# Kernel optimization log

Hardware: AMD Instinct MI355X
Metric: run time of the kernel (lower is better)

The kernel has to match this reference:

```python
import jax, jax.numpy as jnp
import numpy as np

THETA0 = 3.0
THETA = 5.0
BIG = 1e10  # stands in for +inf in the squared-distance transform


def _edt_sq_1d(f):
    # f: [..., n] of squared distances; returns min_j (i-j)^2 + f[j] per i.
    n = f.shape[-1]
    i = jnp.arange(n, dtype=f.dtype)
    d2 = (i[:, None] - i[None, :]) ** 2  # [n, n]
    return jnp.min(f[..., None, :] + d2, axis=-1)


def _edt(mask):
    # Exact Euclidean distance from each voxel to the nearest zero of `mask`
    # (matches scipy.ndimage.distance_transform_edt on a binary mask),
    # via the separable squared-distance transform applied axis by axis.
    f = jnp.where(mask > 0.5, jnp.asarray(BIG, mask.dtype), jnp.asarray(0.0, mask.dtype))
    for ax in range(1, mask.ndim):  # skip batch axis 0
        f = jnp.moveaxis(_edt_sq_1d(jnp.moveaxis(f, ax, -1)), -1, ax)
    return jnp.sqrt(f)


def setup_inputs() -> dict:
    key = jax.random.key(0)
    k1, k2 = jax.random.split(key)
    B, D, H, W = 2, 64, 96, 96
    pred = jax.random.uniform(k1, (B, D, H, W), dtype=jnp.float32)  # probabilities
    target = jax.random.randint(k2, (B, D, H, W), 0, 2).astype(jnp.float32)  # binary mask
    return {"pred": pred, "target": target}


def reference(pred, target):
    # Signed distance phi = dist_to_foreground_boundary framework: 
    # dist_pos = EDT(target) (distance to nearest background voxel),
    # dist_neg = EDT(1 - target).
    dist_pos = _edt(target)
    dist_neg = _edt(1.0 - target)
    a = jnp.abs(dist_neg - dist_pos)
    w = jnp.where(
        a <= THETA0,
        1.0,
        jnp.where(a >= THETA, 0.0, 1.0 - (a - THETA0) / (THETA - THETA0)),
    )
    w = jax.lax.stop_gradient(w)  # original computes weights from detached numpy target

    # binary_cross_entropy with torch's log clamp at -100
    log_p = jnp.clip(jnp.log(pred), -100.0)
    log_1mp = jnp.clip(jnp.log(1.0 - pred), -100.0)
    bce = -(target * log_p + (1.0 - target) * log_1mp)  # [B, D, H, W]

    num = jnp.sum(bce * w, axis=(1, 2, 3))
    den = jnp.sum(w, axis=(1, 2, 3)) + 1e-5
    return jnp.mean(num / den)
```

## Files before the change

kernel.cpp:

```cpp
#include <hip/hip_runtime.h>
#include <math.h>

#define BDIM 2
#define DDIM 64
#define HDIM 96
#define WDIM 96

#define DT 8
#define HT 8
#define WT 32
#define DH 16
#define HH 16
#define NROWS (DH * HH)
#define NBLK  (BDIM * (DDIM / DT) * (HDIM / HT) * (WDIM / WT))

__global__ void init_acc(float* __restrict__ acc) {
    if (threadIdx.x < 4) acc[threadIdx.x] = 0.0f;
    if (threadIdx.x == 4) ((int*)acc)[4] = 0;
}

__device__ __forceinline__ unsigned vminu4(unsigned a, unsigned b) {
    unsigned c = ((a | 0x80808080u) - b) & 0x80808080u;
    unsigned m = (c - (c >> 7)) | c;
    return a ^ ((a ^ b) & m);
}

__device__ __forceinline__ unsigned shiftw(unsigned lo, unsigned hi, int t) {
#if __has_builtin(__builtin_amdgcn_alignbyte)
    return __builtin_amdgcn_alignbyte(hi, lo, t);
#else
    return (lo >> (8 * t)) | (hi << (32 - 8 * t));
#endif
}

__device__ __forceinline__ unsigned wpass_quad(unsigned W0, unsigned W1, unsigned W2) {
    unsigned m = 0x19191919u - W1 * 25u;
    unsigned u08 = W0 | W2;
    m = vminu4(m, 0x19191919u - u08 * 9u);
    unsigned u17 = shiftw(W0, W1, 1) | shiftw(W1, W2, 3);
    m = vminu4(m, 0x19191919u - u17 * 16u);
    unsigned u26 = shiftw(W0, W1, 2) | shiftw(W1, W2, 2);
    m = vminu4(m, 0x19191919u - u26 * 21u);
    unsigned u35 = shiftw(W0, W1, 3) | shiftw(W1, W2, 1);
    m = vminu4(m, 0x19191919u - u35 * 24u);
    return m;
}

__global__ __launch_bounds__(256) void boundary_fused(const float* __restrict__ pred,
                                                      const float* __restrict__ target,
                                                      float* __restrict__ acc,
                                                      float* __restrict__ out) {
    __shared__ unsigned fgm[NROWS * 10];
    __shared__ unsigned bgm[NROWS * 10];
    __shared__ unsigned swp[NROWS * 8];
    __shared__ unsigned swn[NROWS * 8];
    __shared__ float rsum[8];
    unsigned* whp = fgm;
    unsigned* whn = bgm;

    const int tid = threadIdx.x;
    int x = blockIdx.x;
    const int wt = x % 3;  x /= 3;
    const int ht = x % 12; x /= 12;
    const int dt = x % 8;
    const int b  = x / 8;
    const int d0 = dt * DT, h0 = ht * HT, w0 = wt * WT;

    #pragma unroll
    for (int k = 0; k < 10; ++k) {
        const int idx = tid + 256 * k;
        const int row = idx / 10;
        const int q   = idx - row * 10;
        const int dr = row >> 4, hr = row & 15;
        const int d = d0 - 4 + dr, h = h0 - 4 + hr;
        const int wb = w0 - 4 + 4 * q;
        unsigned fgw = 0u, bgw = 0u;
        if ((unsigned)d < DDIM && (unsigned)h < HDIM && (unsigned)wb < WDIM) {
            const float4 v = *(const float4*)(target +
                ((size_t)(b * DDIM + d) * HDIM + h) * WDIM + wb);
            fgw = (unsigned)(v.x > 0.5f)        | ((unsigned)(v.y > 0.5f) << 8) |
                  ((unsigned)(v.z > 0.5f) << 16) | ((unsigned)(v.w > 0.5f) << 24);
            bgw = fgw ^ 0x01010101u;
        }
        fgm[row * 10 + q] = fgw;
        bgm[row * 10 + q] = bgw;
    }
    __syncthreads();

    {
        const int qp = tid & 7;
        const int rb = tid >> 3;
        #pragma unroll
        for (int k = 0; k < 8; ++k) {
            const int row  = rb + 32 * k;
            const int base = row * 10 + qp;
            swn[row * 8 + qp] = wpass_quad(fgm[base], fgm[base + 1], fgm[base + 2]);
            swp[row * 8 + qp] = wpass_quad(bgm[base], bgm[base + 1], bgm[base + 2]);
        }
    }
    __syncthreads();

    #pragma unroll
    for (int k = 0; k < 4; ++k) {
        const int g  = tid + 256 * k;
        const int q  = g & 7;
        const int hh = (g >> 3) & 7;
        const int dr = g >> 6;
        unsigned p = 0x19191919u, n = 0x19191919u;
        #pragma unroll
        for (int t = 0; t < 9; ++t) {
            const unsigned add = (unsigned)((t - 4) * (t - 4)) * 0x01010101u;
            const int src = (dr * HH + hh + t) * 8 + q;
            p = vminu4(p, swp[src] + add);
            n = vminu4(n, swn[src] + add);
        }
        whp[(dr * HT + hh) * 8 + q] = p;
        whn[(dr * HT + hh) * 8 + q] = n;
    }
    __syncthreads();

    float num = 0.f, den = 0.f;
    #pragma unroll
    for (int k = 0; k < 2; ++k) {
        const int g  = tid + 256 * k;
        const int q  = g & 7;
        const int hh = (g >> 3) & 7;
        const int di = g >> 6;
        unsigned p = 0x19191919u, n = 0x19191919u;
        #pragma unroll
        for (int t = 0; t < 9; ++t) {
            const unsigned add = (unsigned)((t - 4) * (t - 4)) * 0x01010101u;
            const int src = ((di + t) * HT + hh) * 8 + q;
            p = vminu4(p, whp[src] + add);
            n = vminu4(n, whn[src] + add);
        }
        const size_t gg = ((size_t)(b * DDIM + d0 + di) * HDIM + h0 + hh) * WDIM
                        + w0 + q * 4;
        const float4 pr = *(const float4*)(pred + gg);
        const float4 tg = *(const float4*)(target + gg);
        #pragma unroll
        for (int j = 0; j < 4; ++j) {
            const float pv = (float)((p >> (8 * j)) & 0xFFu);
            const float nv = (float)((n >> (8 * j)) & 0xFFu);
            const float prj = j == 0 ? pr.x : j == 1 ? pr.y : j == 2 ? pr.z : pr.w;
            const float tgj = j == 0 ? tg.x : j == 1 ? tg.y : j == 2 ? tg.z : tg.w;
            const float dp = sqrtf(pv);
            const float dn = sqrtf(nv);
            const float a  = fabsf(dn - dp);
            float w;
            if (a <= 3.0f)      w = 1.0f;
            else if (a >= 5.0f) w = 0.0f;
            else                w = 1.0f - (a - 3.0f) * 0.5f;
            const float lp  = fmaxf(logf(prj), -100.0f);
            const float l1  = fmaxf(logf(1.0f - prj), -100.0f);
            const float bce = -(tgj * lp + (1.0f - tgj) * l1);
            num += bce * w;
            den += w;
        }
    }

    for (int off = 32; off > 0; off >>= 1) {
        num += __shfl_down(num, off);
        den += __shfl_down(den, off);
    }
    if ((tid & 63) == 0) {
        rsum[tid >> 6]       = num;
        rsum[4 + (tid >> 6)] = den;
    }
    __syncthreads();
    if (tid == 0) {
        float ns = rsum[0] + rsum[1] + rsum[2] + rsum[3];
        float ds = rsum[4] + rsum[5] + rsum[6] + rsum[7];
        atomicAdd(&acc[b], ns);
        atomicAdd(&acc[2 + b], ds);
        __threadfence();
        int done = atomicAdd((int*)acc + 4, 1);
        if (done == NBLK - 1) {
            __threadfence();
            float n0  = atomicAdd(&acc[0], 0.0f);
            float n1  = atomicAdd(&acc[1], 0.0f);
            float d0_ = atomicAdd(&acc[2], 0.0f);
            float d1_ = atomicAdd(&acc[3], 0.0f);
            out[0] = 0.5f * (n0 / (d0_ + 1e-5f) + n1 / (d1_ + 1e-5f));
        }
    }
}

extern "C" void kernel_launch(void* const* d_in, const int* in_sizes, int n_in,
                              void* d_out, int out_size, void* d_ws, size_t ws_size,
                              hipStream_t stream) {
    const float* pred   = (const float*)d_in[0];
    const float* target = (const float*)d_in[1];
    float* acc = (float*)d_ws;
    float* out = (float*)d_out;

    init_acc<<<1, 64, 0, stream>>>(acc);
    boundary_fused<<<NBLK, 256, 0, stream>>>(pred, target, acc, out);
}
```

Before: 94.66 us.

## Repack distance maps as 16-bit pos/neg pairs with per-row register W-pass

Each thread now loads one whole input row into registers and runs the width pass there, so the byte-mask shared arrays and one barrier go away. The results are stored as interleaved 16-bit positive/negative pairs, and the H and D passes use packed u16 min instead of the SWAR byte-min emulation. The final stage switches from float4 per-thread loads to one element per thread, coalesced across 32 columns. This removes shared-memory round trips and bit-trick ALU work, at the cost of more per-thread H/D iterations and scalar global loads.

```diff
diff --git a/kernel.cpp b/kernel.cpp
--- a/kernel.cpp
+++ b/kernel.cpp
@@ -12,7 +12,10 @@
 #define DH 16
 #define HH 16
 #define NROWS (DH * HH)
+#define SWSTR 36
 #define NBLK  (BDIM * (DDIM / DT) * (HDIM / HT) * (WDIM / WT))
+
+typedef unsigned short ushort2v __attribute__((ext_vector_type(2)));
 
 __global__ void init_acc(float* __restrict__ acc) {
     if (threadIdx.x < 4) acc[threadIdx.x] = 0.0f;
@@ -23,6 +26,12 @@
     unsigned c = ((a | 0x80808080u) - b) & 0x80808080u;
     unsigned m = (c - (c >> 7)) | c;
     return a ^ ((a ^ b) & m);
+}
+
+__device__ __forceinline__ unsigned pkmin(unsigned a, unsigned b) {
+    ushort2v r = __builtin_elementwise_min(__builtin_bit_cast(ushort2v, a),
+                                           __builtin_bit_cast(ushort2v, b));
+    return __builtin_bit_cast(unsigned, r);
 }
 
 __device__ __forceinline__ unsigned shiftw(unsigned lo, unsigned hi, int t) {
@@ -50,113 +59,99 @@
                                                       const float* __restrict__ target,
                                                       float* __restrict__ acc,
                                                       float* __restrict__ out) {
-    __shared__ unsigned fgm[NROWS * 10];
-    __shared__ unsigned bgm[NROWS * 10];
-    __shared__ unsigned swp[NROWS * 8];
-    __shared__ unsigned swn[NROWS * 8];
+    __shared__ __align__(16) unsigned swpn[NROWS * SWSTR];
+    __shared__ unsigned whpn[DH * HT * WT];
     __shared__ float rsum[8];
-    unsigned* whp = fgm;
-    unsigned* whn = bgm;
 
     const int tid = threadIdx.x;
     int x = blockIdx.x;
     const int wt = x % 3;  x /= 3;
     const int ht = x % 12; x /= 12;
     const int dt = x % 8;
-    const int b  = x / 8;
+    const int bi = x / 8;
     const int d0 = dt * DT, h0 = ht * HT, w0 = wt * WT;
 
-    #pragma unroll
-    for (int k = 0; k < 10; ++k) {
-        const int idx = tid + 256 * k;
-        const int row = idx / 10;
-        const int q   = idx - row * 10;
-        const int dr = row >> 4, hr = row & 15;
+    {
+        const int r  = tid;
+        const int dr = r >> 4, hr = r & 15;
         const int d = d0 - 4 + dr, h = h0 - 4 + hr;
-        const int wb = w0 - 4 + 4 * q;
-        unsigned fgw = 0u, bgw = 0u;
-        if ((unsigned)d < DDIM && (unsigned)h < HDIM && (unsigned)wb < WDIM) {
-            const float4 v = *(const float4*)(target +
-                ((size_t)(b * DDIM + d) * HDIM + h) * WDIM + wb);
-            fgw = (unsigned)(v.x > 0.5f)        | ((unsigned)(v.y > 0.5f) << 8) |
-                  ((unsigned)(v.z > 0.5f) << 16) | ((unsigned)(v.w > 0.5f) << 24);
-            bgw = fgw ^ 0x01010101u;
+        const bool rowvalid = ((unsigned)d < DDIM) && ((unsigned)h < HDIM);
+        const unsigned rv = rowvalid ? 0x01010101u : 0u;
+        const float* rowp = target + ((size_t)(bi * DDIM + d) * HDIM + h) * WDIM + (w0 - 4);
+
+        unsigned Wf[10], Wb[10];
+        #pragma unroll
+        for (int q = 0; q < 10; ++q) {
+            unsigned vbq = 0x01010101u;
+            if (q == 0 && wt == 0) vbq = 0u;
+            if (q == 9 && wt == 2) vbq = 0u;
+            unsigned fg = 0u;
+            if (rowvalid && vbq) {
+                const float4 v = *(const float4*)(rowp + 4 * q);
+                fg = (unsigned)(v.x > 0.5f)         | ((unsigned)(v.y > 0.5f) << 8) |
+                     ((unsigned)(v.z > 0.5f) << 16) | ((unsigned)(v.w > 0.5f) << 24);
+            }
+            Wf[q] = fg;
+            Wb[q] = (fg ^ 0x01010101u) & vbq & rv;
         }
-        fgm[row * 10 + q] = fgw;
-        bgm[row * 10 + q] = bgw;
-    }
-    __syncthreads();
-
-    {
-        const int qp = tid & 7;
-        const int rb = tid >> 3;
         #pragma unroll
-        for (int k = 0; k < 8; ++k) {
-            const int row  = rb + 32 * k;
-            const int base = row * 10 + qp;
-            swn[row * 8 + qp] = wpass_quad(fgm[base], fgm[base + 1], fgm[base + 2]);
-            swp[row * 8 + qp] = wpass_quad(bgm[base], bgm[base + 1], bgm[base + 2]);
+        for (int q = 0; q < 8; ++q) {
+            const unsigned nb = wpass_quad(Wf[q], Wf[q + 1], Wf[q + 2]);
+            const unsigned pb = wpass_quad(Wb[q], Wb[q + 1], Wb[q + 2]);
+            uint4 e;
+            e.x = (pb & 0xFFu)         | ((nb & 0xFFu) << 16);
+            e.y = ((pb >> 8) & 0xFFu)  | (((nb >> 8) & 0xFFu) << 16);
+            e.z = ((pb >> 16) & 0xFFu) | (((nb >> 16) & 0xFFu) << 16);
+            e.w = (pb >> 24)           | ((nb >> 24) << 16);
+            *(uint4*)&swpn[r * SWSTR + 4 * q] = e;
         }
     }
     __syncthreads();
 
     #pragma unroll
-    for (int k = 0; k < 4; ++k) {
-        const int g  = tid + 256 * k;
-        const int q  = g & 7;
-        const int hh = (g >> 3) & 7;
-        const int dr = g >> 6;
-        unsigned p = 0x19191919u, n = 0x19191919u;
+    for (int k = 0; k < 16; ++k) {
+        const int idx = tid + 256 * k;
+        const int c   = idx & 31;
+        const int hh  = (idx >> 5) & 7;
+        const int dr  = idx >> 8;
+        unsigned a = 0x00190019u;
         #pragma unroll
         for (int t = 0; t < 9; ++t) {
-            const unsigned add = (unsigned)((t - 4) * (t - 4)) * 0x01010101u;
-            const int src = (dr * HH + hh + t) * 8 + q;
-            p = vminu4(p, swp[src] + add);
-            n = vminu4(n, swn[src] + add);
+            const unsigned v = swpn[(dr * HH + hh + t) * SWSTR + c];
+            a = pkmin(a, v + (unsigned)((t - 4) * (t - 4)) * 0x00010001u);
         }
-        whp[(dr * HT + hh) * 8 + q] = p;
-        whn[(dr * HT + hh) * 8 + q] = n;
+        whpn[(dr * HT + hh) * WT + c] = a;
     }
     __syncthreads();
 
     float num = 0.f, den = 0.f;
     #pragma unroll
-    for (int k = 0; k < 2; ++k) {
-        const int g  = tid + 256 * k;
-        const int q  = g & 7;
-        const int hh = (g >> 3) & 7;
-        const int di = g >> 6;
-        unsigned p = 0x19191919u, n = 0x19191919u;
+    for (int k = 0; k < 8; ++k) {
+        const int idx = tid + 256 * k;
+        const int c   = idx & 31;
+        const int hh  = (idx >> 5) & 7;
+        const int di  = idx >> 8;
+        unsigned a = 0x00190019u;
         #pragma unroll
         for (int t = 0; t < 9; ++t) {
-            const unsigned add = (unsigned)((t - 4) * (t - 4)) * 0x01010101u;
-            const int src = ((di + t) * HT + hh) * 8 + q;
-            p = vminu4(p, whp[src] + add);
-            n = vminu4(n, whn[src] + add);
+            const unsigned v = whpn[((di + t) * HT + hh) * WT + c];
+            a = pkmin(a, v + (unsigned)((t - 4) * (t - 4)) * 0x00010001u);
         }
-        const size_t gg = ((size_t)(b * DDIM + d0 + di) * HDIM + h0 + hh) * WDIM
-                        + w0 + q * 4;
-        const float4 pr = *(const float4*)(pred + gg);
-        const float4 tg = *(const float4*)(target + gg);
-        #pragma unroll
-        for (int j = 0; j < 4; ++j) {
-            const float pv = (float)((p >> (8 * j)) & 0xFFu);
-            const float nv = (float)((n >> (8 * j)) & 0xFFu);
-            const float prj = j == 0 ? pr.x : j == 1 ? pr.y : j == 2 ? pr.z : pr.w;
-            const float tgj = j == 0 ? tg.x : j == 1 ? tg.y : j == 2 ? tg.z : tg.w;
-            const float dp = sqrtf(pv);
-            const float dn = sqrtf(nv);
-            const float a  = fabsf(dn - dp);
-            float w;
-            if (a <= 3.0f)      w = 1.0f;
-            else if (a >= 5.0f) w = 0.0f;
-            else                w = 1.0f - (a - 3.0f) * 0.5f;
-            const float lp  = fmaxf(logf(prj), -100.0f);
-            const float l1  = fmaxf(logf(1.0f - prj), -100.0f);
-            const float bce = -(tgj * lp + (1.0f - tgj) * l1);
-            num += bce * w;
-            den += w;
-        }
+        const size_t g = ((size_t)(bi * DDIM + d0 + di) * HDIM + h0 + hh) * WDIM + w0 + c;
+        const float pr = pred[g];
+        const float tg = target[g];
+        const float dp = sqrtf((float)(a & 0xFFFFu));
+        const float dn = sqrtf((float)(a >> 16));
+        const float aa = fabsf(dn - dp);
+        float w;
+        if (aa <= 3.0f)      w = 1.0f;
+        else if (aa >= 5.0f) w = 0.0f;
+        else                 w = 1.0f - (aa - 3.0f) * 0.5f;
+        const float lp  = fmaxf(logf(pr), -100.0f);
+        const float l1  = fmaxf(logf(1.0f - pr), -100.0f);
+        const float bce = -(tg * lp + (1.0f - tg) * l1);
+        num += bce * w;
+        den += w;
     }
 
     for (int off = 32; off > 0; off >>= 1) {
@@ -171,8 +166,8 @@
     if (tid == 0) {
         float ns = rsum[0] + rsum[1] + rsum[2] + rsum[3];
         float ds = rsum[4] + rsum[5] + rsum[6] + rsum[7];
-        atomicAdd(&acc[b], ns);
-        atomicAdd(&acc[2 + b], ds);
+        atomicAdd(&acc[bi], ns);
+        atomicAdd(&acc[2 + bi], ds);
         __threadfence();
         int done = atomicAdd((int*)acc + 4, 1);
         if (done == NBLK - 1) {
```

New measurement: 94.96 us. No clear change (+0.3%).
